# Optimization experiments

Hardware: AMD Instinct MI355X
Metric: run time of the kernel (lower is better)

## Reference

```python
import jax, jax.numpy as jnp
import numpy as np

HEADS = 4
SIZE = 3


def setup_inputs() -> dict:
    key = jax.random.key(0)
    ks = jax.random.split(key, 8)
    B, C, D, H, W = 2, 64, 24, 24, 24
    s = 1.0 / np.sqrt(C)
    x = jax.random.normal(ks[0], (B, C, D, H, W), jnp.float32)
    cemb = jax.random.normal(ks[1], (B, C), jnp.float32)
    Wq = jax.random.normal(ks[2], (C, C), jnp.float32) * s
    bq = jax.random.normal(ks[3], (C,), jnp.float32) * 0.01
    Wk = jax.random.normal(ks[4], (C, C), jnp.float32) * s
    bk = jax.random.normal(ks[5], (C,), jnp.float32) * 0.01
    Wv = jax.random.normal(ks[6], (C, C), jnp.float32) * s
    bv = jax.random.normal(ks[7], (C,), jnp.float32) * 0.01
    return {"x": x, "cemb": cemb, "Wq": Wq, "bq": bq, "Wk": Wk, "bk": bk, "Wv": Wv, "bv": bv}


def _unfold(t, size, heads):
    # t: (B, D, H, W, C) -> (B, D*H*W, heads, size^3, C//heads), zero padded borders
    B, D, H, W, C = t.shape
    pad = size // 2
    tp = jnp.pad(t, ((0, 0), (pad, pad), (pad, pad), (pad, pad), (0, 0)))
    # depth shift outermost, then height, then width (matches torch unfold order)
    patches = jnp.stack(
        [tp[:, i:i + D, j:j + H, l:l + W, :]
         for i in range(size) for j in range(size) for l in range(size)],
        axis=4)  # (B, D, H, W, ws, C)
    ws = size ** 3
    hd = C // heads
    return patches.reshape(B, D * H * W, ws, heads, hd).transpose(0, 1, 3, 2, 4)


def reference(x, cemb, Wq, bq, Wk, bk, Wv, bv):
    # x: (B, C, D, H, W); cemb unused by the original forward
    B, C, D, H, W = x.shape
    heads, size = HEADS, SIZE
    hd = C // heads
    xc = jnp.transpose(x, (0, 2, 3, 4, 1))  # (B, D, H, W, C)
    q = xc @ Wq.T + bq
    k = xc @ Wk.T + bk
    v = xc @ Wv.T + bv
    kw = _unfold(k, size, heads)  # (B, N, h, ws, hd)
    vw = _unfold(v, size, heads)
    qh = q.reshape(B, D * H * W, heads, 1, hd) * (hd ** -0.5)
    attn = jnp.einsum('bnhqd,bnhkd->bnhqk', qh, kw)  # (B, N, h, 1, ws)
    attn = jax.nn.softmax(attn, axis=-1)
    h = jnp.einsum('bnhqk,bnhkd->bnhqd', attn, vw).reshape(B, D, H, W, C)
    out = xc + h
    return jnp.transpose(out, (0, 4, 1, 2, 3))
```

## Files before the change

### kernel.cpp

```cpp
#include <hip/hip_runtime.h>

#define NV 13824
#define CCH 64
#define NB 2

__global__ __launch_bounds__(256) void qkv_kernel(
    const float* __restrict__ x,
    const float* __restrict__ Wq, const float* __restrict__ bq,
    const float* __restrict__ Wk, const float* __restrict__ bk,
    const float* __restrict__ Wv, const float* __restrict__ bv,
    float* __restrict__ qo, float* __restrict__ ko, float* __restrict__ vo)
{
    __shared__ float sb[3][64][20];

    const int t    = threadIdx.x;
    const int bid  = blockIdx.x;
    const int lb   = (bid & 7) * 216 + (bid >> 3);
    const int tile = lb >> 2;
    const int cqg  = lb & 3;
    const int wid  = t >> 6;
    const int lane = t & 63;

    const int gr0 = tile * 64;
    const int b   = gr0 / NV;
    const int nn  = gr0 - b * NV;
    const int n   = nn + lane;
    const int c0  = __builtin_amdgcn_readfirstlane(cqg * 16 + wid * 4);

    const float* xb = x + (size_t)b * CCH * NV + n;

    float xr[64];
    #pragma unroll
    for (int k = 0; k < 64; ++k) xr[k] = xb[(size_t)k * NV];

    const float* const Ws[3] = {Wq, Wk, Wv};
    const float* const bs[3] = {bq, bk, bv};

    #pragma unroll
    for (int m = 0; m < 3; ++m) {
        const float sc = (m == 0) ? 0.25f : 1.0f;
        #pragma unroll
        for (int j = 0; j < 4; ++j) {
            const float* row = Ws[m] + (size_t)(c0 + j) * 64;
            float a = bs[m][c0 + j];
            #pragma unroll
            for (int k4 = 0; k4 < 16; ++k4) {
                const float4 wv = *(const float4*)(row + k4 * 4);
                a += xr[k4 * 4 + 0] * wv.x + xr[k4 * 4 + 1] * wv.y
                   + xr[k4 * 4 + 2] * wv.z + xr[k4 * 4 + 3] * wv.w;
            }
            sb[m][lane][wid * 4 + j] = a * sc;
        }
    }
    __syncthreads();

    const int v = t >> 2;
    const int i = t & 3;
    float* const outs[3] = {qo, ko, vo};
    #pragma unroll
    for (int m = 0; m < 3; ++m) {
        const float4 o4 = *(const float4*)(&sb[m][v][i * 4]);
        *(float4*)(outs[m] + (size_t)(gr0 + v) * 64 + cqg * 16 + i * 4) = o4;
    }
}

__global__ __launch_bounds__(256) void attn_kernel(
    const float* __restrict__ x,
    const float* __restrict__ qw,
    const float* __restrict__ kw,
    const float* __restrict__ vw,
    float* __restrict__ out)
{
    __shared__ float so[32][65];

    const int t    = threadIdx.x;
    const int bid  = blockIdx.x;
    const int lb   = (bid & 7) * 108 + (bid >> 3);
    const int half = t & 1;
    const int head = (t >> 1) & 3;
    const int vb   = t >> 3;
    const int n0g  = lb * 32;
    const int gr   = n0g + vb;
    const int b    = gr / NV;
    const int n    = gr - b * NV;
    const int d    = n / 576;
    const int rem  = n - d * 576;
    const int r    = rem / 24;
    const int w    = rem - r * 24;
    const int coff = head * 16 + half * 8;

    int   idx[27];
    float msk[27];
    #pragma unroll
    for (int i3 = 0; i3 < 3; ++i3)
    #pragma unroll
    for (int j3 = 0; j3 < 3; ++j3)
    #pragma unroll
    for (int l3 = 0; l3 < 3; ++l3) {
        const int dd = d + i3 - 1;
        const int rr = r + j3 - 1;
        const int ww = w + l3 - 1;
        const bool ok = ((unsigned)dd < 24u) & ((unsigned)rr < 24u) & ((unsigned)ww < 24u);
        const int jj = (i3 * 3 + j3) * 3 + l3;
        idx[jj] = ok ? ((dd * 24 + rr) * 24 + ww) : n;
        msk[jj] = ok ? 1.f : 0.f;
    }

    const float4* qp = (const float4*)(qw + (size_t)gr * 64 + coff);
    const float4 q0 = qp[0], q1 = qp[1];

    const float* kbase = kw + (size_t)b * NV * 64 + coff;

    float logit[27];
    #pragma unroll
    for (int j = 0; j < 27; ++j) {
        const float4* kp = (const float4*)(kbase + (size_t)idx[j] * 64);
        const float4 k0 = kp[0], k1 = kp[1];
        float a;
        a  = q0.x * k0.x + q0.y * k0.y + q0.z * k0.z + q0.w * k0.w;
        a += q1.x * k1.x + q1.y * k1.y + q1.z * k1.z + q1.w * k1.w;
        logit[j] = a * msk[j];
    }
    #pragma unroll
    for (int j = 0; j < 27; ++j)
        logit[j] += __shfl_xor(logit[j], 1, 64);

    float ssum = 0.f;
    #pragma unroll
    for (int j = 0; j < 27; ++j) {
        const float e = __expf(logit[j]);
        logit[j] = e;
        ssum += e;
    }
    const float inv = 1.f / ssum;

    float a0=0.f,a1=0.f,a2=0.f,a3=0.f,a4=0.f,a5=0.f,a6=0.f,a7=0.f;
    const float* vbase = vw + (size_t)b * NV * 64 + coff;
    #pragma unroll
    for (int j = 0; j < 27; ++j) {
        const float p = logit[j] * msk[j];
        const float4* vp = (const float4*)(vbase + (size_t)idx[j] * 64);
        const float4 v0 = vp[0], v1 = vp[1];
        a0 += p * v0.x; a1 += p * v0.y; a2 += p * v0.z; a3 += p * v0.w;
        a4 += p * v1.x; a5 += p * v1.y; a6 += p * v1.z; a7 += p * v1.w;
    }

    so[vb][coff + 0] = a0 * inv;  so[vb][coff + 1] = a1 * inv;
    so[vb][coff + 2] = a2 * inv;  so[vb][coff + 3] = a3 * inv;
    so[vb][coff + 4] = a4 * inv;  so[vb][coff + 5] = a5 * inv;
    so[vb][coff + 6] = a6 * inv;  so[vb][coff + 7] = a7 * inv;
    __syncthreads();

    const int vv = t & 31;
    const int cg = t >> 5;
    const int bs = n0g / NV;
    const int nb0 = n0g - bs * NV;
    const float* xb = x   + (size_t)bs * CCH * NV + nb0 + vv;
    float*       ob = out + (size_t)bs * CCH * NV + nb0 + vv;
    #pragma unroll
    for (int i = 0; i < 8; ++i) {
        const int c = cg * 8 + i;
        ob[(size_t)c * NV] = xb[(size_t)c * NV] + so[vv][c];
    }
}

extern "C" void kernel_launch(void* const* d_in, const int* in_sizes, int n_in,
                              void* d_out, int out_size, void* d_ws, size_t ws_size,
                              hipStream_t stream) {
    const float* x  = (const float*)d_in[0];
    const float* Wq = (const float*)d_in[2];
    const float* bq = (const float*)d_in[3];
    const float* Wk = (const float*)d_in[4];
    const float* bk = (const float*)d_in[5];
    const float* Wv = (const float*)d_in[6];
    const float* bv = (const float*)d_in[7];
    float* out = (float*)d_out;

    float* ws = (float*)d_ws;
    const size_t RC = (size_t)NB * NV * CCH;
    float* q = ws;
    float* k = ws + RC;
    float* v = ws + 2 * RC;

    const int nrows = NB * NV;

    qkv_kernel<<<nrows / 16, 256, 0, stream>>>(x, Wq, bq, Wk, bk, Wv, bv, q, k, v);
    attn_kernel<<<nrows / 32, 256, 0, stream>>>(x, q, k, v, out);
}
```

Measured before the change: 112.8 us.

## Tile attention into 4x4x4 voxel blocks with K/V halos staged in LDS

The attention kernel now assigns each block a 4x4x4 voxel tile and a pair of heads, cooperatively loads the 6x6x6 K and V halo plus Q into shared memory with an XOR swizzle, and reads the 27-neighbour window from LDS instead of gathering it repeatedly from global memory. Zero padding is materialised in LDS, so the per-neighbour mask disappears. This is meant to cut redundant global and L2 traffic from overlapping windows. In exchange it uses much more LDS per block (about 63 KB), which limits occupancy, and the output store becomes less coalesced because of the 3D tile indexing.

```diff
diff --git a/kernel.cpp b/kernel.cpp
--- a/kernel.cpp
+++ b/kernel.cpp
@@ -71,55 +71,77 @@
     const float* __restrict__ vw,
     float* __restrict__ out)
 {
-    __shared__ float so[32][65];
+    __shared__ float4 sK[216 * 8];
+    __shared__ float4 sV[216 * 8];
+    __shared__ float4 sQ[64 * 8];
+    __shared__ float  so[64][33];
 
     const int t    = threadIdx.x;
     const int bid  = blockIdx.x;
     const int lb   = (bid & 7) * 108 + (bid >> 3);
+    const int hp   = lb & 1;
+    const int tile = lb >> 1;
+    const int b    = tile / 216;
+    const int tl   = tile - b * 216;
+    const int d0   = (tl / 36) * 4;
+    const int r0   = ((tl % 36) / 6) * 4;
+    const int w0   = (tl % 6) * 4;
+
+    const float* kwb = kw + (size_t)b * NV * 64 + hp * 32;
+    const float* vwb = vw + (size_t)b * NV * 64 + hp * 32;
+    const float* qwb = qw + (size_t)b * NV * 64 + hp * 32;
+
+    for (int g = t; g < 216 * 8; g += 256) {
+        const int row = g >> 3;
+        const int j   = g & 7;
+        const int hz  = row / 36;
+        const int hy  = (row % 36) / 6;
+        const int hx  = row % 6;
+        const int dd  = d0 - 1 + hz;
+        const int rr  = r0 - 1 + hy;
+        const int ww  = w0 - 1 + hx;
+        const bool ok = ((unsigned)dd < 24u) & ((unsigned)rr < 24u) & ((unsigned)ww < 24u);
+        const int n   = ok ? ((dd * 24 + rr) * 24 + ww) : 0;
+        float4 kv = *(const float4*)(kwb + (size_t)n * 64 + j * 4);
+        float4 vv = *(const float4*)(vwb + (size_t)n * 64 + j * 4);
+        if (!ok) { kv = make_float4(0.f, 0.f, 0.f, 0.f); vv = kv; }
+        const int dst = row * 8 + (j ^ (row & 7));
+        sK[dst] = kv;
+        sV[dst] = vv;
+    }
+    for (int g = t; g < 64 * 8; g += 256) {
+        const int row = g >> 3;
+        const int j   = g & 7;
+        const int n   = ((d0 + (row >> 4)) * 24 + (r0 + ((row >> 2) & 3))) * 24
+                        + (w0 + (row & 3));
+        sQ[row * 8 + (j ^ (row & 7))] =
+            *(const float4*)(qwb + (size_t)n * 64 + j * 4);
+    }
+    __syncthreads();
+
+    const int vox  = t >> 2;
+    const int hh   = (t >> 1) & 1;
     const int half = t & 1;
-    const int head = (t >> 1) & 3;
-    const int vb   = t >> 3;
-    const int n0g  = lb * 32;
-    const int gr   = n0g + vb;
-    const int b    = gr / NV;
-    const int n    = gr - b * NV;
-    const int d    = n / 576;
-    const int rem  = n - d * 576;
-    const int r    = rem / 24;
-    const int w    = rem - r * 24;
-    const int coff = head * 16 + half * 8;
-
-    int   idx[27];
-    float msk[27];
+    const int j0   = hh * 4 + half * 2;
+    const int lz   = vox >> 4, ly = (vox >> 2) & 3, lx = vox & 3;
+
+    const float4 q0 = sQ[vox * 8 + (j0 ^ (vox & 7))];
+    const float4 q1 = sQ[vox * 8 + ((j0 + 1) ^ (vox & 7))];
+
+    float logit[27];
     #pragma unroll
     for (int i3 = 0; i3 < 3; ++i3)
     #pragma unroll
     for (int j3 = 0; j3 < 3; ++j3)
     #pragma unroll
     for (int l3 = 0; l3 < 3; ++l3) {
-        const int dd = d + i3 - 1;
-        const int rr = r + j3 - 1;
-        const int ww = w + l3 - 1;
-        const bool ok = ((unsigned)dd < 24u) & ((unsigned)rr < 24u) & ((unsigned)ww < 24u);
-        const int jj = (i3 * 3 + j3) * 3 + l3;
-        idx[jj] = ok ? ((dd * 24 + rr) * 24 + ww) : n;
-        msk[jj] = ok ? 1.f : 0.f;
-    }
-
-    const float4* qp = (const float4*)(qw + (size_t)gr * 64 + coff);
-    const float4 q0 = qp[0], q1 = qp[1];
-
-    const float* kbase = kw + (size_t)b * NV * 64 + coff;
-
-    float logit[27];
-    #pragma unroll
-    for (int j = 0; j < 27; ++j) {
-        const float4* kp = (const float4*)(kbase + (size_t)idx[j] * 64);
-        const float4 k0 = kp[0], k1 = kp[1];
+        const int hidx = (lz + i3) * 36 + (ly + j3) * 6 + (lx + l3);
+        const float4 k0 = sK[hidx * 8 + (j0 ^ (hidx & 7))];
+        const float4 k1 = sK[hidx * 8 + ((j0 + 1) ^ (hidx & 7))];
         float a;
         a  = q0.x * k0.x + q0.y * k0.y + q0.z * k0.z + q0.w * k0.w;
         a += q1.x * k1.x + q1.y * k1.y + q1.z * k1.z + q1.w * k1.w;
-        logit[j] = a * msk[j];
+        logit[(i3 * 3 + j3) * 3 + l3] = a;
     }
     #pragma unroll
     for (int j = 0; j < 27; ++j)
@@ -135,32 +157,38 @@
     const float inv = 1.f / ssum;
 
     float a0=0.f,a1=0.f,a2=0.f,a3=0.f,a4=0.f,a5=0.f,a6=0.f,a7=0.f;
-    const float* vbase = vw + (size_t)b * NV * 64 + coff;
-    #pragma unroll
-    for (int j = 0; j < 27; ++j) {
-        const float p = logit[j] * msk[j];
-        const float4* vp = (const float4*)(vbase + (size_t)idx[j] * 64);
-        const float4 v0 = vp[0], v1 = vp[1];
+    #pragma unroll
+    for (int i3 = 0; i3 < 3; ++i3)
+    #pragma unroll
+    for (int j3 = 0; j3 < 3; ++j3)
+    #pragma unroll
+    for (int l3 = 0; l3 < 3; ++l3) {
+        const int hidx = (lz + i3) * 36 + (ly + j3) * 6 + (lx + l3);
+        const float p = logit[(i3 * 3 + j3) * 3 + l3];
+        const float4 v0 = sV[hidx * 8 + (j0 ^ (hidx & 7))];
+        const float4 v1 = sV[hidx * 8 + ((j0 + 1) ^ (hidx & 7))];
         a0 += p * v0.x; a1 += p * v0.y; a2 += p * v0.z; a3 += p * v0.w;
         a4 += p * v1.x; a5 += p * v1.y; a6 += p * v1.z; a7 += p * v1.w;
     }
 
-    so[vb][coff + 0] = a0 * inv;  so[vb][coff + 1] = a1 * inv;
-    so[vb][coff + 2] = a2 * inv;  so[vb][coff + 3] = a3 * inv;
-    so[vb][coff + 4] = a4 * inv;  so[vb][coff + 5] = a5 * inv;
-    so[vb][coff + 6] = a6 * inv;  so[vb][coff + 7] = a7 * inv;
+    const int cb = hh * 16 + half * 8;
+    so[vox][cb + 0] = a0 * inv;  so[vox][cb + 1] = a1 * inv;
+    so[vox][cb + 2] = a2 * inv;  so[vox][cb + 3] = a3 * inv;
+    so[vox][cb + 4] = a4 * inv;  so[vox][cb + 5] = a5 * inv;
+    so[vox][cb + 6] = a6 * inv;  so[vox][cb + 7] = a7 * inv;
     __syncthreads();
 
-    const int vv = t & 31;
-    const int cg = t >> 5;
-    const int bs = n0g / NV;
-    const int nb0 = n0g - bs * NV;
-    const float* xb = x   + (size_t)bs * CCH * NV + nb0 + vv;
-    float*       ob = out + (size_t)bs * CCH * NV + nb0 + vv;
+    const int vv = t & 63;
+    const int cg = t >> 6;
+    const int n2 = ((d0 + (vv >> 4)) * 24 + (r0 + ((vv >> 2) & 3))) * 24
+                   + (w0 + (vv & 3));
+    const float* xb = x   + (size_t)b * CCH * NV + n2;
+    float*       ob = out + (size_t)b * CCH * NV + n2;
     #pragma unroll
     for (int i = 0; i < 8; ++i) {
-        const int c = cg * 8 + i;
-        ob[(size_t)c * NV] = xb[(size_t)c * NV] + so[vv][c];
+        const int c  = cg * 8 + i;
+        const int gc = hp * 32 + c;
+        ob[(size_t)gc * NV] = xb[(size_t)gc * NV] + so[vv][c];
     }
 }
 
@@ -185,5 +213,5 @@
     const int nrows = NB * NV;
 
     qkv_kernel<<<nrows / 16, 256, 0, stream>>>(x, Wq, bq, Wk, bk, Wv, bv, q, k, v);
-    attn_kernel<<<nrows / 32, 256, 0, stream>>>(x, q, k, v, out);
+    attn_kernel<<<864, 256, 0, stream>>>(x, q, k, v, out);
 }
```

New measurement: 116.5 us. +3.3%, slower.

## Retile QKV projection as register-blocked GEMM with weights staged in LDS

Applied to the files above, without the earlier changes.

The QKV projection kernel is restructured so each block handles 256 voxels by 32 output channels of one of Q/K/V. The pre-scaled weight slice and bias are staged in shared memory, and each thread computes a 4-voxel by 8-channel register tile using float4 loads of x. This replaces the old scheme where every thread held all 64 input channels in registers and re-read weight rows from global memory, aiming to cut register pressure and improve reuse. Results are transposed through a padded LDS buffer so the channel-last stores to q/k/v stay coalesced. The cost is more LDS traffic and one extra barrier, and each block now reads x for only 32 of the 192 output channels, so x is re-read six times.

```diff
diff --git a/kernel.cpp b/kernel.cpp
--- a/kernel.cpp
+++ b/kernel.cpp
@@ -11,56 +11,87 @@
     const float* __restrict__ Wv, const float* __restrict__ bv,
     float* __restrict__ qo, float* __restrict__ ko, float* __restrict__ vo)
 {
-    __shared__ float sb[3][64][20];
-
-    const int t    = threadIdx.x;
-    const int bid  = blockIdx.x;
-    const int lb   = (bid & 7) * 216 + (bid >> 3);
-    const int tile = lb >> 2;
-    const int cqg  = lb & 3;
-    const int wid  = t >> 6;
-    const int lane = t & 63;
-
-    const int gr0 = tile * 64;
-    const int b   = gr0 / NV;
-    const int nn  = gr0 - b * NV;
-    const int n   = nn + lane;
-    const int c0  = __builtin_amdgcn_readfirstlane(cqg * 16 + wid * 4);
-
-    const float* xb = x + (size_t)b * CCH * NV + n;
-
-    float xr[64];
-    #pragma unroll
-    for (int k = 0; k < 64; ++k) xr[k] = xb[(size_t)k * NV];
-
-    const float* const Ws[3] = {Wq, Wk, Wv};
-    const float* const bs[3] = {bq, bk, bv};
-
-    #pragma unroll
-    for (int m = 0; m < 3; ++m) {
-        const float sc = (m == 0) ? 0.25f : 1.0f;
+    __shared__ float  sW[32 * 64];
+    __shared__ float  sB2[32];
+    __shared__ float4 sO[32 * 65];
+
+    const int t   = threadIdx.x;
+    const int bid = blockIdx.x;
+    const int lb  = (bid & 7) * 81 + (bid >> 3);
+    const int oc  = lb % 6;
+    const int nch = lb / 6;
+    const int m   = oc >> 1;
+    const int ch0 = (oc & 1) * 32;
+    const int b   = nch / 54;
+    const int nn  = (nch - b * 54) * 256;
+    const float sc = (m == 0) ? 0.25f : 1.0f;
+
+    {
+        const float* const Ws[3] = {Wq, Wk, Wv};
+        const float* const bs[3] = {bq, bk, bv};
+        const float4* src = (const float4*)(Ws[m] + ch0 * 64);
+        float4* dst = (float4*)sW;
         #pragma unroll
-        for (int j = 0; j < 4; ++j) {
-            const float* row = Ws[m] + (size_t)(c0 + j) * 64;
-            float a = bs[m][c0 + j];
+        for (int g = 0; g < 2; ++g) {
+            float4 wv4 = src[g * 256 + t];
+            wv4.x *= sc; wv4.y *= sc; wv4.z *= sc; wv4.w *= sc;
+            dst[g * 256 + t] = wv4;
+        }
+        if (t < 32) sB2[t] = bs[m][ch0 + t] * sc;
+    }
+    __syncthreads();
+
+    const int tn = t & 63;
+    const int tw = t >> 6;
+    const float* xp = x + (size_t)b * CCH * NV + nn + tn * 4;
+    const float4* sW4 = (const float4*)sW;
+
+    float4 acc[8];
+    #pragma unroll
+    for (int i = 0; i < 8; ++i) acc[i] = make_float4(0.f, 0.f, 0.f, 0.f);
+
+    #pragma unroll 4
+    for (int c4 = 0; c4 < 16; ++c4) {
+        float4 w4[8];
+        #pragma unroll
+        for (int i = 0; i < 8; ++i) w4[i] = sW4[(tw * 8 + i) * 16 + c4];
+        #pragma unroll
+        for (int cc = 0; cc < 4; ++cc) {
+            const float4 xv = *(const float4*)(xp + (size_t)(c4 * 4 + cc) * NV);
             #pragma unroll
-            for (int k4 = 0; k4 < 16; ++k4) {
-                const float4 wv = *(const float4*)(row + k4 * 4);
-                a += xr[k4 * 4 + 0] * wv.x + xr[k4 * 4 + 1] * wv.y
-                   + xr[k4 * 4 + 2] * wv.z + xr[k4 * 4 + 3] * wv.w;
+            for (int i = 0; i < 8; ++i) {
+                const float ws = (cc == 0) ? w4[i].x : (cc == 1) ? w4[i].y
+                               : (cc == 2) ? w4[i].z : w4[i].w;
+                acc[i].x += xv.x * ws; acc[i].y += xv.y * ws;
+                acc[i].z += xv.z * ws; acc[i].w += xv.w * ws;
             }
-            sb[m][lane][wid * 4 + j] = a * sc;
         }
     }
+
+    #pragma unroll
+    for (int i = 0; i < 8; ++i) {
+        const int ol = tw * 8 + i;
+        const float bb = sB2[ol];
+        float4 a = acc[i];
+        a.x += bb; a.y += bb; a.z += bb; a.w += bb;
+        sO[ol * 65 + tn] = a;
+    }
     __syncthreads();
 
-    const int v = t >> 2;
-    const int i = t & 3;
     float* const outs[3] = {qo, ko, vo};
-    #pragma unroll
-    for (int m = 0; m < 3; ++m) {
-        const float4 o4 = *(const float4*)(&sb[m][v][i * 4]);
-        *(float4*)(outs[m] + (size_t)(gr0 + v) * 64 + cqg * 16 + i * 4) = o4;
+    const float* sOf = (const float*)sO;
+    float* ob = outs[m] + (size_t)(b * NV + nn) * 64 + ch0;
+    #pragma unroll
+    for (int it = 0; it < 8; ++it) {
+        const int g   = it * 256 + t;
+        const int n   = g >> 3;
+        const int of4 = g & 7;
+        float4 o4;
+        o4.x = sOf[(of4 * 4 + 0) * 260 + n];
+        o4.y = sOf[(of4 * 4 + 1) * 260 + n];
+        o4.z = sOf[(of4 * 4 + 2) * 260 + n];
+        o4.w = sOf[(of4 * 4 + 3) * 260 + n];
+        *(float4*)(ob + (size_t)n * 64 + of4 * 4) = o4;
     }
 }
 
@@ -182,8 +213,6 @@
     float* k = ws + RC;
     float* v = ws + 2 * RC;
 
-    const int nrows = NB * NV;
-
-    qkv_kernel<<<nrows / 16, 256, 0, stream>>>(x, Wq, bq, Wk, bk, Wv, bv, q, k, v);
-    attn_kernel<<<nrows / 32, 256, 0, stream>>>(x, q, k, v, out);
+    qkv_kernel<<<648, 256, 0, stream>>>(x, Wq, bq, Wk, bk, Wv, bv, q, k, v);
+    attn_kernel<<<864, 256, 0, stream>>>(x, q, k, v, out);
 }
```

New measurement: 107.9 us. 4.4% less time.
